# Kernel optimization log

Measured on AMD Instinct MI355X. Metric: run time of the kernel, lower is better.

The kernel has to match this reference:

```python
import jax, jax.numpy as jnp
import numpy as np

M, N, D, P = 1024, 4096, 128, 3072
H = N // D


def setup_inputs() -> dict:
    key = jax.random.key(0)
    ks = jax.random.split(key, 6)
    X = jax.random.normal(ks[0], (M, N), dtype=jnp.float32)
    W_q = jax.random.normal(ks[1], (N, N), dtype=jnp.float32) * 0.02
    W_k = jax.random.normal(ks[2], (N, N), dtype=jnp.float32) * 0.02
    W_v = jax.random.normal(ks[3], (N, N), dtype=jnp.float32) * 0.02
    cache_K = jax.random.normal(ks[4], (H, P, D), dtype=jnp.float32)
    cache_V = jax.random.normal(ks[5], (H, P, D), dtype=jnp.float32)
    return {"X": X, "W_q": W_q, "W_k": W_k, "W_v": W_v,
            "cache_K": cache_K, "cache_V": cache_V}


def _rms_norm(t):
    # RMS over last dim, no eps, no learned scale (matches source)
    var = jnp.mean(t * t, axis=-1, keepdims=True)
    return t * jax.lax.rsqrt(var)


def reference(X, W_q, W_k, W_v, cache_K, cache_V):
    # QKV projections: [M, N] -> [H, M, D]
    q = (X @ W_q).reshape(M, H, D).transpose(1, 0, 2)
    k = (X @ W_k).reshape(M, H, D).transpose(1, 0, 2)
    v = (X @ W_v).reshape(M, H, D).transpose(1, 0, 2)

    q = _rms_norm(q)
    k = _rms_norm(k)

    # KV-cache concat along sequence dim: [H, P+M, D]
    k_cache = jnp.concatenate([cache_K[:, :P, :], k], axis=1)
    v_cache = jnp.concatenate([cache_V[:, :P, :], v], axis=1)

    # Non-causal prefill attention, sm_scale = 1.0
    scores = jnp.einsum('hmd,hnd->hmn', q, k_cache)  # [H, M, P+M]
    attn = jax.nn.softmax(scores, axis=-1)
    out = jnp.einsum('hmn,hnd->hmd', attn, v_cache)  # [H, M, D]

    return out.transpose(1, 0, 2).reshape(M, N)
```

## Files before the change

kernel.cpp:

```cpp
#include <hip/hip_runtime.h>

#define MM 1024
#define NN 4096
#define DD 128
#define HH 32
#define PP 3072
#define LL 4096

typedef __attribute__((ext_vector_type(8))) short short8;
typedef __attribute__((ext_vector_type(4))) float f32x4;

__device__ __forceinline__ float bf2f(short b) {
  union { unsigned u; float f; } c;
  c.u = ((unsigned)(unsigned short)b) << 16;
  return c.f;
}

__device__ __forceinline__ short f2bf(float f) {
  union { float f; unsigned u; } c; c.f = f;
  unsigned r = c.u + 0x7FFFu + ((c.u >> 16) & 1u);
  return (short)(r >> 16);
}

struct bf2 { short hi, lo; };
__device__ __forceinline__ bf2 split2(float x) {
  bf2 r;
  r.hi = f2bf(x);
  r.lo = f2bf(x - bf2f(r.hi));
  return r;
}

__device__ __forceinline__ short8 cvt8(const float* __restrict__ p) {
  const f32x4 a = *(const f32x4*)p;
  const f32x4 b = *(const f32x4*)(p + 4);
  short8 r;
  r[0] = f2bf(a[0]); r[1] = f2bf(a[1]); r[2] = f2bf(a[2]); r[3] = f2bf(a[3]);
  r[4] = f2bf(b[0]); r[5] = f2bf(b[1]); r[6] = f2bf(b[2]); r[7] = f2bf(b[3]);
  return r;
}

__device__ __forceinline__ void gload16(const void* g, void* l) {
  __builtin_amdgcn_global_load_lds(
      (const __attribute__((address_space(1))) void*)g,
      (__attribute__((address_space(3))) void*)l, 16, 0, 0);
}

__global__ __launch_bounds__(256) void split_x(
    const float* __restrict__ in, short* __restrict__ oh,
    short* __restrict__ ol, int n8)
{
  int i = blockIdx.x * blockDim.x + threadIdx.x;
  if (i >= n8) return;
  const float* p = in + (size_t)i * 8;
  f32x4 a = *(const f32x4*)p, b = *(const f32x4*)(p + 4);
  short8 h, l;
  #pragma unroll
  for (int j = 0; j < 4; ++j) {
    bf2 ra = split2(a[j]); h[j] = ra.hi; l[j] = ra.lo;
    bf2 rb = split2(b[j]); h[4 + j] = rb.hi; l[4 + j] = rb.lo;
  }
  *(short8*)(oh + (size_t)i * 8) = h;
  *(short8*)(ol + (size_t)i * 8) = l;
}

__global__ __launch_bounds__(256) void split_w_t(
    const float* __restrict__ W, short* __restrict__ oh,
    short* __restrict__ ol)
{
  const int n0 = blockIdx.x * 256;
  const int k0 = blockIdx.y * 64;
  const int t  = threadIdx.x;
  const int k8 = k0 + ((t >> 5) << 3);
  const int n8 = n0 + ((t & 31) << 3);

  f32x4 xa[8], xb[8];
  #pragma unroll
  for (int r = 0; r < 8; ++r) {
    const float* p = W + (size_t)(k8 + r) * 4096 + n8;
    xa[r] = *(const f32x4*)p;
    xb[r] = *(const f32x4*)(p + 4);
  }
  #pragma unroll
  for (int c = 0; c < 8; ++c) {
    short8 th, tl;
    #pragma unroll
    for (int r = 0; r < 8; ++r) {
      float v = (c < 4) ? xa[r][c] : xb[r][c - 4];
      bf2 s = split2(v);
      th[r] = s.hi; tl[r] = s.lo;
    }
    size_t o = (size_t)(n8 + c) * 4096 + k8;
    *(short8*)(oh + o) = th;
    if (ol) *(short8*)(ol + o) = tl;
  }
}

__global__ __launch_bounds__(256) void gemm_split_bt(
    const short* __restrict__ Ah_g, const short* __restrict__ Al_g,
    const short* __restrict__ Bh_g, const short* __restrict__ Bl_g,
    float* __restrict__ O)
{
  const int n0 = blockIdx.x * 128;
  const int m0 = blockIdx.y * 128;
  const int t  = threadIdx.x;
  const int wave = t >> 6;
  const int lane = t & 63;
  const int ln   = lane & 15;
  const int quad = lane >> 4;
  const int q8   = quad * 8;
  const int wm = (wave >> 1) * 64;
  const int wn = (wave & 1) * 64;
  const int sr = lane >> 3;
  const int sc = (lane & 7) * 8;

  __shared__ short Ash[128 * 64];
  __shared__ short Asl[128 * 64];
  __shared__ short Bsh[128 * 64];
  __shared__ short Bsl[128 * 64];

  f32x4 acc[4][4];
  #pragma unroll
  for (int mi = 0; mi < 4; ++mi)
    #pragma unroll
    for (int ni = 0; ni < 4; ++ni)
      acc[mi][ni] = (f32x4){0.f, 0.f, 0.f, 0.f};

  const size_t a_base = (size_t)(m0 + wave * 32 + sr) * 4096 + sc;
  const size_t b_base = (size_t)(n0 + wave * 32 + sr) * 4096 + sc;
  const int l_base = wave * 32 * 64;

  for (int kt = 0; kt < 4096; kt += 64) {
    #pragma unroll
    for (int i = 0; i < 4; ++i) {
      size_t ao = a_base + kt + (size_t)(i * 8) * 4096;
      size_t bo = b_base + kt + (size_t)(i * 8) * 4096;
      int lo = l_base + i * 8 * 64;
      gload16(Ah_g + ao, Ash + lo);
      gload16(Al_g + ao, Asl + lo);
      gload16(Bh_g + bo, Bsh + lo);
      gload16(Bl_g + bo, Bsl + lo);
    }
    __syncthreads();
    #pragma unroll
    for (int kk = 0; kk < 64; kk += 32) {
      short8 ah[4], al[4], bh[4], bl[4];
      #pragma unroll
      for (int mi = 0; mi < 4; ++mi) {
        int ro = (wm + mi * 16 + ln) * 64 + kk + q8;
        ah[mi] = *(const short8*)(Ash + ro);
        al[mi] = *(const short8*)(Asl + ro);
      }
      #pragma unroll
      for (int ni = 0; ni < 4; ++ni) {
        int ro = (wn + ni * 16 + ln) * 64 + kk + q8;
        bh[ni] = *(const short8*)(Bsh + ro);
        bl[ni] = *(const short8*)(Bsl + ro);
      }
      #pragma unroll
      for (int ni = 0; ni < 4; ++ni)
        #pragma unroll
        for (int mi = 0; mi < 4; ++mi) {
          acc[mi][ni] = __builtin_amdgcn_mfma_f32_16x16x32_bf16(ah[mi], bh[ni], acc[mi][ni], 0, 0, 0);
          acc[mi][ni] = __builtin_amdgcn_mfma_f32_16x16x32_bf16(ah[mi], bl[ni], acc[mi][ni], 0, 0, 0);
          acc[mi][ni] = __builtin_amdgcn_mfma_f32_16x16x32_bf16(al[mi], bh[ni], acc[mi][ni], 0, 0, 0);
        }
    }
    __syncthreads();
  }

  #pragma unroll
  for (int mi = 0; mi < 4; ++mi)
    #pragma unroll
    for (int ni = 0; ni < 4; ++ni)
      #pragma unroll
      for (int r = 0; r < 4; ++r) {
        int row = m0 + wm + mi * 16 + quad * 4 + r;
        int col = n0 + wn + ni * 16 + ln;
        O[(size_t)row * 4096 + col] = acc[mi][ni][r];
      }
}

__global__ __launch_bounds__(256) void gemm_bf16_bt(
    const short* __restrict__ Ah_g, const short* __restrict__ Bh_g,
    short* __restrict__ Ov)
{
  const int n0 = blockIdx.x * 128;
  const int m0 = blockIdx.y * 128;
  const int t  = threadIdx.x;
  const int wave = t >> 6;
  const int lane = t & 63;
  const int ln   = lane & 15;
  const int quad = lane >> 4;
  const int q8   = quad * 8;
  const int wm = (wave >> 1) * 64;
  const int wn = (wave & 1) * 64;
  const int sr = lane >> 3;
  const int sc = (lane & 7) * 8;

  __shared__ short Ash[128 * 64];
  __shared__ short Bsh[128 * 64];

  f32x4 acc[4][4];
  #pragma unroll
  for (int mi = 0; mi < 4; ++mi)
    #pragma unroll
    for (int ni = 0; ni < 4; ++ni)
      acc[mi][ni] = (f32x4){0.f, 0.f, 0.f, 0.f};

  const size_t a_base = (size_t)(m0 + wave * 32 + sr) * 4096 + sc;
  const size_t b_base = (size_t)(n0 + wave * 32 + sr) * 4096 + sc;
  const int l_base = wave * 32 * 64;

  for (int kt = 0; kt < 4096; kt += 64) {
    #pragma unroll
    for (int i = 0; i < 4; ++i) {
      size_t ao = a_base + kt + (size_t)(i * 8) * 4096;
      size_t bo = b_base + kt + (size_t)(i * 8) * 4096;
      int lo = l_base + i * 8 * 64;
      gload16(Ah_g + ao, Ash + lo);
      gload16(Bh_g + bo, Bsh + lo);
    }
    __syncthreads();
    #pragma unroll
    for (int kk = 0; kk < 64; kk += 32) {
      short8 ah[4], bh[4];
      #pragma unroll
      for (int mi = 0; mi < 4; ++mi)
        ah[mi] = *(const short8*)(Ash + (wm + mi * 16 + ln) * 64 + kk + q8);
      #pragma unroll
      for (int ni = 0; ni < 4; ++ni)
        bh[ni] = *(const short8*)(Bsh + (wn + ni * 16 + ln) * 64 + kk + q8);
      #pragma unroll
      for (int ni = 0; ni < 4; ++ni)
        #pragma unroll
        for (int mi = 0; mi < 4; ++mi)
          acc[mi][ni] = __builtin_amdgcn_mfma_f32_16x16x32_bf16(ah[mi], bh[ni], acc[mi][ni], 0, 0, 0);
    }
    __syncthreads();
  }

  #pragma unroll
  for (int mi = 0; mi < 4; ++mi)
    #pragma unroll
    for (int ni = 0; ni < 4; ++ni)
      #pragma unroll
      for (int r = 0; r < 4; ++r) {
        int row = m0 + wm + mi * 16 + quad * 4 + r;
        int col = n0 + wn + ni * 16 + ln;
        Ov[(size_t)row * 4096 + col] = f2bf(acc[mi][ni][r]);
      }
}

__global__ __launch_bounds__(256) void rmsnorm_f32(
    float* __restrict__ Q, float* __restrict__ K)
{
  float* __restrict__ buf = (blockIdx.y == 0) ? Q : K;
  const int m = blockIdx.x;
  const int t = threadIdx.x;
  const int head = t >> 3, li = t & 7;
  size_t base = (size_t)m * 4096 + head * 128 + li * 16;

  f32x4 a[4];
  float ss = 0.f;
  #pragma unroll
  for (int i = 0; i < 4; ++i) {
    a[i] = *(const f32x4*)(buf + base + i * 4);
    #pragma unroll
    for (int j = 0; j < 4; ++j) ss += a[i][j] * a[i][j];
  }
  #pragma unroll
  for (int d = 1; d < 8; d <<= 1) ss += __shfl_xor(ss, d, 64);
  float scale = rsqrtf(ss * (1.0f / 128.0f));
  #pragma unroll
  for (int i = 0; i < 4; ++i) {
    #pragma unroll
    for (int j = 0; j < 4; ++j) a[i][j] *= scale;
    *(f32x4*)(buf + base + i * 4) = a[i];
  }
}

__global__ __launch_bounds__(256) void attn(
    const float* __restrict__ Qf,
    const float* __restrict__ Kf,
    const short* __restrict__ Vb,
    const float* __restrict__ cK,
    const float* __restrict__ cV,
    float* __restrict__ Out)
{
  const int h  = blockIdx.y;
  const int m0 = blockIdx.x * 64;
  const int t  = threadIdx.x;
  const int w    = t >> 6;
  const int lane = t & 63;
  const int ln   = lane & 15;
  const int quad = lane >> 4;
  const int q8   = quad * 8;

  __shared__ short k_hi[64 * 136];
  __shared__ short k_lo[64 * 136];
  __shared__ short v_s[64 * 136];
  __shared__ short p_s[64 * 72];
  __shared__ float a_l[64], l_l[64];

  short8 qh[4], ql[4];
  {
    int qrow = m0 + w * 16 + ln;
    #pragma unroll
    for (int dc = 0; dc < 4; ++dc) {
      const float* qp = Qf + (size_t)qrow * 4096 + h * 128 + dc * 32 + q8;
      f32x4 a = *(const f32x4*)qp, b = *(const f32x4*)(qp + 4);
      #pragma unroll
      for (int j = 0; j < 4; ++j) {
        bf2 ra = split2(a[j]); qh[dc][j] = ra.hi; ql[dc][j] = ra.lo;
        bf2 rb = split2(b[j]); qh[dc][4 + j] = rb.hi; ql[dc][4 + j] = rb.lo;
      }
    }
  }

  float m_st[4], l_st[4];
  #pragma unroll
  for (int r = 0; r < 4; ++r) { m_st[r] = -1e30f; l_st[r] = 0.f; }

  f32x4 oacc[4][2];
  #pragma unroll
  for (int ms = 0; ms < 4; ++ms)
    #pragma unroll
    for (int i = 0; i < 2; ++i)
      oacc[ms][i] = (f32x4){0.f, 0.f, 0.f, 0.f};

  for (int kb = 0; kb < LL; kb += 64) {
    #pragma unroll
    for (int i = 0; i < 2; ++i) {
      int kr = i * 32 + (t >> 3);
      int g  = kb + kr;
      int dc = (t & 7) * 16;
      const float* ks = (g < PP)
          ? cK + ((size_t)h * PP + g) * 128 + dc
          : Kf + (size_t)(g - PP) * 4096 + h * 128 + dc;
      f32x4 x0 = *(const f32x4*)ks,       x1 = *(const f32x4*)(ks + 4);
      f32x4 x2 = *(const f32x4*)(ks + 8), x3 = *(const f32x4*)(ks + 12);
      short8 h0, l0, h1, l1;
      #pragma unroll
      for (int j = 0; j < 4; ++j) {
        bf2 r0 = split2(x0[j]); h0[j] = r0.hi; l0[j] = r0.lo;
        bf2 r1 = split2(x1[j]); h0[4 + j] = r1.hi; l0[4 + j] = r1.lo;
        bf2 r2 = split2(x2[j]); h1[j] = r2.hi; l1[j] = r2.lo;
        bf2 r3 = split2(x3[j]); h1[4 + j] = r3.hi; l1[4 + j] = r3.lo;
      }
      *(short8*)(k_hi + kr * 136 + dc)     = h0;
      *(short8*)(k_hi + kr * 136 + dc + 8) = h1;
      *(short8*)(k_lo + kr * 136 + dc)     = l0;
      *(short8*)(k_lo + kr * 136 + dc + 8) = l1;

      short8 v0, v1;
      if (g < PP) {
        const float* vs = cV + ((size_t)h * PP + g) * 128 + dc;
        v0 = cvt8(vs); v1 = cvt8(vs + 8);
      } else {
        const short* vp = Vb + (size_t)(g - PP) * 4096 + h * 128 + dc;
        v0 = *(const short8*)vp; v1 = *(const short8*)(vp + 8);
      }
      int b0 = ((dc >> 3) + 0) ^ (kr >> 3);
      int b1 = ((dc >> 3) + 1) ^ (kr >> 3);
      *(short8*)(v_s + kr * 136 + b0 * 8) = v0;
      *(short8*)(v_s + kr * 136 + b1 * 8) = v1;
    }
    __syncthreads();

    f32x4 sacc[4];
    #pragma unroll
    for (int ni = 0; ni < 4; ++ni) sacc[ni] = (f32x4){0.f, 0.f, 0.f, 0.f};
    #pragma unroll
    for (int ni = 0; ni < 4; ++ni) {
      #pragma unroll
      for (int dc = 0; dc < 4; ++dc) {
        int ro = (ni * 16 + ln) * 136 + dc * 32 + q8;
        short8 kh = *(const short8*)(k_hi + ro);
        short8 kl = *(const short8*)(k_lo + ro);
        sacc[ni] = __builtin_amdgcn_mfma_f32_16x16x32_bf16(qh[dc], kh, sacc[ni], 0, 0, 0);
        sacc[ni] = __builtin_amdgcn_mfma_f32_16x16x32_bf16(qh[dc], kl, sacc[ni], 0, 0, 0);
        sacc[ni] = __builtin_amdgcn_mfma_f32_16x16x32_bf16(ql[dc], kh, sacc[ni], 0, 0, 0);
      }
    }

    float alpha[4];
    #pragma unroll
    for (int rr = 0; rr < 4; ++rr) {
      float mx = fmaxf(fmaxf(sacc[0][rr], sacc[1][rr]),
                       fmaxf(sacc[2][rr], sacc[3][rr]));
      #pragma unroll
      for (int d = 1; d < 16; d <<= 1) mx = fmaxf(mx, __shfl_xor(mx, d, 64));
      float mn = fmaxf(m_st[rr], mx);
      alpha[rr] = __expf(m_st[rr] - mn);
      float p0 = __expf(sacc[0][rr] - mn);
      float p1 = __expf(sacc[1][rr] - mn);
      float p2 = __expf(sacc[2][rr] - mn);
      float p3 = __expf(sacc[3][rr] - mn);
      float s = p0 + p1 + p2 + p3;
      #pragma unroll
      for (int d = 1; d < 16; d <<= 1) s += __shfl_xor(s, d, 64);
      l_st[rr] = l_st[rr] * alpha[rr] + s;
      m_st[rr] = mn;
      int prow = (w * 16 + quad * 4 + rr) * 72;
      p_s[prow + 0 * 16 + ln] = f2bf(p0);
      p_s[prow + 1 * 16 + ln] = f2bf(p1);
      p_s[prow + 2 * 16 + ln] = f2bf(p2);
      p_s[prow + 3 * 16 + ln] = f2bf(p3);
    }
    if (ln == 0) {
      #pragma unroll
      for (int rr = 0; rr < 4; ++rr) a_l[w * 16 + quad * 4 + rr] = alpha[rr];
    }
    __syncthreads();

    #pragma unroll
    for (int ms = 0; ms < 4; ++ms) {
      f32x4 av = *(const f32x4*)(a_l + ms * 16 + quad * 4);
      #pragma unroll
      for (int i = 0; i < 2; ++i)
        #pragma unroll
        for (int r = 0; r < 4; ++r) oacc[ms][i][r] *= av[r];
    }
    #pragma unroll
    for (int kk = 0; kk < 64; kk += 32) {
      short8 vf[2];
      #pragma unroll
      for (int i = 0; i < 2; ++i) {
        int cbb = (w * 2 + i) * 2 + (ln >> 3);
        #pragma unroll
        for (int j = 0; j < 8; ++j) {
          int k = kk + q8 + j;
          vf[i][j] = v_s[k * 136 + ((cbb ^ (k >> 3)) << 3) + (ln & 7)];
        }
      }
      #pragma unroll
      for (int ms = 0; ms < 4; ++ms) {
        short8 pf = *(const short8*)(p_s + (ms * 16 + ln) * 72 + kk + q8);
        #pragma unroll
        for (int i = 0; i < 2; ++i)
          oacc[ms][i] = __builtin_amdgcn_mfma_f32_16x16x32_bf16(pf, vf[i], oacc[ms][i], 0, 0, 0);
      }
    }
    __syncthreads();
  }

  if (ln == 0) {
    #pragma unroll
    for (int rr = 0; rr < 4; ++rr) l_l[w * 16 + quad * 4 + rr] = l_st[rr];
  }
  __syncthreads();

  #pragma unroll
  for (int ms = 0; ms < 4; ++ms) {
    f32x4 lv = *(const f32x4*)(l_l + ms * 16 + quad * 4);
    #pragma unroll
    for (int i = 0; i < 2; ++i) {
      int col = h * 128 + (w * 2 + i) * 16 + ln;
      #pragma unroll
      for (int r = 0; r < 4; ++r) {
        int row = m0 + ms * 16 + quad * 4 + r;
        Out[(size_t)row * 4096 + col] = oacc[ms][i][r] / lv[r];
      }
    }
  }
}

extern "C" void kernel_launch(void* const* d_in, const int* in_sizes, int n_in,
                              void* d_out, int out_size, void* d_ws, size_t ws_size,
                              hipStream_t stream) {
  const float* X  = (const float*)d_in[0];
  const float* Wq = (const float*)d_in[1];
  const float* Wk = (const float*)d_in[2];
  const float* Wv = (const float*)d_in[3];
  const float* cK = (const float*)d_in[4];
  const float* cV = (const float*)d_in[5];
  float* out = (float*)d_out;

  const size_t E  = (size_t)MM * NN;
  const size_t WE = (size_t)NN * NN;
  short* Xh  = (short*)d_ws;
  short* Xl  = Xh + E;
  short* Vb  = Xl + E;
  float* Qf  = (float*)(Vb + E);
  float* Kf  = Qf + E;
  short* Wth = (short*)(Kf + E);
  short* Wtl = Wth + WE;

  {
    int n8 = (int)(E / 8);
    split_x<<<n8 / 256, 256, 0, stream>>>(X, Xh, Xl, n8);
  }

  dim3 gw(NN / 256, NN / 64);
  dim3 gg(NN / 128, MM / 128);

  split_w_t<<<gw, 256, 0, stream>>>(Wq, Wth, Wtl);
  gemm_split_bt<<<gg, 256, 0, stream>>>(Xh, Xl, Wth, Wtl, Qf);

  split_w_t<<<gw, 256, 0, stream>>>(Wk, Wth, Wtl);
  gemm_split_bt<<<gg, 256, 0, stream>>>(Xh, Xl, Wth, Wtl, Kf);

  split_w_t<<<gw, 256, 0, stream>>>(Wv, Wth, nullptr);
  gemm_bf16_bt<<<gg, 256, 0, stream>>>(Xh, Wth, Vb);

  dim3 gn(MM, 2);
  rmsnorm_f32<<<gn, 256, 0, stream>>>(Qf, Kf);

  dim3 ga(MM / 64, HH);
  attn<<<ga, 256, 0, stream>>>(Qf, Kf, Vb, cK, cV, out);
}
```

Before: 1.023 ms.

## Precompute split-bf16 K and transposed V buffers, load tiles via direct LDS loads

Adds prep kernels that convert K (cache plus new rows) into swizzled hi/lo bf16 arrays and V into pre-transposed, swizzled bf16 tiles once per head, instead of every attention block redoing the fp32-to-bf16 split and the transpose for each key tile. The attention loop then streams ready-made tiles into LDS with 16-byte global-to-LDS loads, reads V fragments as single vector loads instead of scalar gathers, and raises wave priority around the MFMA sections. The cost is two extra kernel launches, extra global traffic to write and re-read the prepared buffers, and workspace aliasing that reuses the weight and Kf regions.

```diff
diff --git a/kernel.cpp b/kernel.cpp
--- a/kernel.cpp
+++ b/kernel.cpp
@@ -279,12 +279,79 @@
   }
 }
 
+__global__ __launch_bounds__(256) void prep_k(
+    const float* __restrict__ Kf, const float* __restrict__ cK,
+    short* __restrict__ Khi, short* __restrict__ Klo)
+{
+  const int h  = blockIdx.y;
+  const int k0 = blockIdx.x * 64;
+  const int t  = threadIdx.x;
+  const int d0 = (t & 7) * 16;
+  #pragma unroll
+  for (int i = 0; i < 2; ++i) {
+    int key = k0 + i * 32 + (t >> 3);
+    const float* src = (key < PP)
+        ? cK + ((size_t)h * PP + key) * 128 + d0
+        : Kf + (size_t)(key - PP) * 4096 + h * 128 + d0;
+    f32x4 x0 = *(const f32x4*)src,       x1 = *(const f32x4*)(src + 4);
+    f32x4 x2 = *(const f32x4*)(src + 8), x3 = *(const f32x4*)(src + 12);
+    short8 h0, l0, h1, l1;
+    #pragma unroll
+    for (int j = 0; j < 4; ++j) {
+      bf2 r0 = split2(x0[j]); h0[j] = r0.hi; l0[j] = r0.lo;
+      bf2 r1 = split2(x1[j]); h0[4 + j] = r1.hi; l0[4 + j] = r1.lo;
+      bf2 r2 = split2(x2[j]); h1[j] = r2.hi; l1[j] = r2.lo;
+      bf2 r3 = split2(x3[j]); h1[4 + j] = r3.hi; l1[4 + j] = r3.lo;
+    }
+    size_t row = ((size_t)h * 4096 + key) * 128;
+    int s  = key & 7;
+    int b0 = (t & 7) * 2, b1 = b0 + 1;
+    *(short8*)(Khi + row + ((b0 ^ s) << 3)) = h0;
+    *(short8*)(Khi + row + ((b1 ^ s) << 3)) = h1;
+    *(short8*)(Klo + row + ((b0 ^ s) << 3)) = l0;
+    *(short8*)(Klo + row + ((b1 ^ s) << 3)) = l1;
+  }
+}
+
+__global__ __launch_bounds__(256) void prep_v(
+    const short* __restrict__ Vb, const float* __restrict__ cV,
+    short* __restrict__ Vtt)
+{
+  const int h    = blockIdx.y;
+  const int k0   = blockIdx.x * 128;
+  const int t    = threadIdx.x;
+  const int kb_g = (k0 >> 3) + (t >> 4);
+  const int db   = t & 15;
+  const int key0 = kb_g * 8;
+
+  short8 row[8];
+  if (key0 < PP) {
+    #pragma unroll
+    for (int r = 0; r < 8; ++r)
+      row[r] = cvt8(cV + ((size_t)h * PP + key0 + r) * 128 + db * 8);
+  } else {
+    #pragma unroll
+    for (int r = 0; r < 8; ++r)
+      row[r] = *(const short8*)(Vb + (size_t)(key0 + r - PP) * 4096 + h * 128 + db * 8);
+  }
+
+  const int tile = kb_g >> 3, kbt = kb_g & 7;
+  size_t tb = ((size_t)h * 64 + tile) * 8192;
+  #pragma unroll
+  for (int c = 0; c < 8; ++c) {
+    int d = db * 8 + c;
+    short8 o;
+    #pragma unroll
+    for (int r = 0; r < 8; ++r) o[r] = row[r][c];
+    *(short8*)(Vtt + tb + d * 64 + ((kbt ^ c) << 3)) = o;
+  }
+}
+
 __global__ __launch_bounds__(256) void attn(
     const float* __restrict__ Qf,
-    const float* __restrict__ Kf,
-    const short* __restrict__ Vb,
-    const float* __restrict__ cK,
-    const float* __restrict__ cV,
+    const short* __restrict__ Khi,
+    const short* __restrict__ Klo,
+    const short* __restrict__ Vtt,
     float* __restrict__ Out)
 {
   const int h  = blockIdx.y;
@@ -296,9 +363,9 @@
   const int quad = lane >> 4;
   const int q8   = quad * 8;
 
-  __shared__ short k_hi[64 * 136];
-  __shared__ short k_lo[64 * 136];
-  __shared__ short v_s[64 * 136];
+  __shared__ short k_hi[64 * 128];
+  __shared__ short k_lo[64 * 128];
+  __shared__ short v_t[128 * 64];
   __shared__ short p_s[64 * 72];
   __shared__ float a_l[64], l_l[64];
 
@@ -328,53 +395,31 @@
     for (int i = 0; i < 2; ++i)
       oacc[ms][i] = (f32x4){0.f, 0.f, 0.f, 0.f};
 
+  const size_t khead = (size_t)h * 4096 * 128;
+  const size_t vhead = (size_t)h * 64 * 8192;
+
   for (int kb = 0; kb < LL; kb += 64) {
-    #pragma unroll
-    for (int i = 0; i < 2; ++i) {
-      int kr = i * 32 + (t >> 3);
-      int g  = kb + kr;
-      int dc = (t & 7) * 16;
-      const float* ks = (g < PP)
-          ? cK + ((size_t)h * PP + g) * 128 + dc
-          : Kf + (size_t)(g - PP) * 4096 + h * 128 + dc;
-      f32x4 x0 = *(const f32x4*)ks,       x1 = *(const f32x4*)(ks + 4);
-      f32x4 x2 = *(const f32x4*)(ks + 8), x3 = *(const f32x4*)(ks + 12);
-      short8 h0, l0, h1, l1;
-      #pragma unroll
-      for (int j = 0; j < 4; ++j) {
-        bf2 r0 = split2(x0[j]); h0[j] = r0.hi; l0[j] = r0.lo;
-        bf2 r1 = split2(x1[j]); h0[4 + j] = r1.hi; l0[4 + j] = r1.lo;
-        bf2 r2 = split2(x2[j]); h1[j] = r2.hi; l1[j] = r2.lo;
-        bf2 r3 = split2(x3[j]); h1[4 + j] = r3.hi; l1[4 + j] = r3.lo;
-      }
-      *(short8*)(k_hi + kr * 136 + dc)     = h0;
-      *(short8*)(k_hi + kr * 136 + dc + 8) = h1;
-      *(short8*)(k_lo + kr * 136 + dc)     = l0;
-      *(short8*)(k_lo + kr * 136 + dc + 8) = l1;
-
-      short8 v0, v1;
-      if (g < PP) {
-        const float* vs = cV + ((size_t)h * PP + g) * 128 + dc;
-        v0 = cvt8(vs); v1 = cvt8(vs + 8);
-      } else {
-        const short* vp = Vb + (size_t)(g - PP) * 4096 + h * 128 + dc;
-        v0 = *(const short8*)vp; v1 = *(const short8*)(vp + 8);
-      }
-      int b0 = ((dc >> 3) + 0) ^ (kr >> 3);
-      int b1 = ((dc >> 3) + 1) ^ (kr >> 3);
-      *(short8*)(v_s + kr * 136 + b0 * 8) = v0;
-      *(short8*)(v_s + kr * 136 + b1 * 8) = v1;
+    const size_t kt = khead + (size_t)kb * 128;
+    const size_t vt = vhead + (size_t)(kb >> 6) * 8192;
+    #pragma unroll
+    for (int i = 0; i < 4; ++i) {
+      int lo = i * 2048 + w * 512;
+      gload16(Khi + kt + lo + lane * 8, k_hi + lo);
+      gload16(Klo + kt + lo + lane * 8, k_lo + lo);
+      gload16(Vtt + vt + lo + lane * 8, v_t + lo);
     }
     __syncthreads();
 
     f32x4 sacc[4];
     #pragma unroll
     for (int ni = 0; ni < 4; ++ni) sacc[ni] = (f32x4){0.f, 0.f, 0.f, 0.f};
+    __builtin_amdgcn_s_setprio(1);
     #pragma unroll
     for (int ni = 0; ni < 4; ++ni) {
+      const int r = ni * 16 + ln;
       #pragma unroll
       for (int dc = 0; dc < 4; ++dc) {
-        int ro = (ni * 16 + ln) * 136 + dc * 32 + q8;
+        int ro = r * 128 + (((dc * 4 + quad) ^ (r & 7)) << 3);
         short8 kh = *(const short8*)(k_hi + ro);
         short8 kl = *(const short8*)(k_lo + ro);
         sacc[ni] = __builtin_amdgcn_mfma_f32_16x16x32_bf16(qh[dc], kh, sacc[ni], 0, 0, 0);
@@ -382,6 +427,7 @@
         sacc[ni] = __builtin_amdgcn_mfma_f32_16x16x32_bf16(ql[dc], kh, sacc[ni], 0, 0, 0);
       }
     }
+    __builtin_amdgcn_s_setprio(0);
 
     float alpha[4];
     #pragma unroll
@@ -426,13 +472,11 @@
       short8 vf[2];
       #pragma unroll
       for (int i = 0; i < 2; ++i) {
-        int cbb = (w * 2 + i) * 2 + (ln >> 3);
-        #pragma unroll
-        for (int j = 0; j < 8; ++j) {
-          int k = kk + q8 + j;
-          vf[i][j] = v_s[k * 136 + ((cbb ^ (k >> 3)) << 3) + (ln & 7)];
-        }
-      }
+        int d = (w * 2 + i) * 16 + ln;
+        int ro = d * 64 + ((((kk + q8) >> 3) ^ (d & 7)) << 3);
+        vf[i] = *(const short8*)(v_t + ro);
+      }
+      __builtin_amdgcn_s_setprio(1);
       #pragma unroll
       for (int ms = 0; ms < 4; ++ms) {
         short8 pf = *(const short8*)(p_s + (ms * 16 + ln) * 72 + kk + q8);
@@ -440,6 +484,7 @@
         for (int i = 0; i < 2; ++i)
           oacc[ms][i] = __builtin_amdgcn_mfma_f32_16x16x32_bf16(pf, vf[i], oacc[ms][i], 0, 0, 0);
       }
+      __builtin_amdgcn_s_setprio(0);
     }
     __syncthreads();
   }
@@ -476,18 +521,21 @@
   const float* cV = (const float*)d_in[5];
   float* out = (float*)d_out;
 
-  const size_t E  = (size_t)MM * NN;
-  const size_t WE = (size_t)NN * NN;
-  short* Xh  = (short*)d_ws;
-  short* Xl  = Xh + E;
-  short* Vb  = Xl + E;
-  float* Qf  = (float*)(Vb + E);
-  float* Kf  = Qf + E;
-  short* Wth = (short*)(Kf + E);
-  short* Wtl = Wth + WE;
+  const size_t MB = 1u << 20;
+  char* w = (char*)d_ws;
+  float* Qf  = (float*)(w);
+  float* Kf  = (float*)(w + 16 * MB);
+  short* Xh  = (short*)(w + 32 * MB);
+  short* Xl  = (short*)(w + 40 * MB);
+  short* Vb  = (short*)(w + 48 * MB);
+  short* Wth = (short*)(w + 56 * MB);
+  short* Wtl = (short*)(w + 88 * MB);
+  short* Khi = (short*)(w + 56 * MB);
+  short* Klo = (short*)(w + 88 * MB);
+  short* Vtt = (short*)(w + 16 * MB);
 
   {
-    int n8 = (int)(E / 8);
+    int n8 = (int)((size_t)MM * NN / 8);
     split_x<<<n8 / 256, 256, 0, stream>>>(X, Xh, Xl, n8);
   }
 
@@ -506,6 +554,11 @@
   dim3 gn(MM, 2);
   rmsnorm_f32<<<gn, 256, 0, stream>>>(Qf, Kf);
 
+  dim3 gk(LL / 64, HH);
+  prep_k<<<gk, 256, 0, stream>>>(Kf, cK, Khi, Klo);
+  dim3 gv(LL / 128, HH);
+  prep_v<<<gv, 256, 0, stream>>>(Vb, cV, Vtt);
+
   dim3 ga(MM / 64, HH);
-  attn<<<ga, 256, 0, stream>>>(Qf, Kf, Vb, cK, cV, out);
-}
+  attn<<<ga, 256, 0, stream>>>(Qf, Khi, Klo, Vtt, out);
+}
```

New measurement: 918.7 us. 1.11x faster.
